# Kernel optimization log

Hardware: AMD Instinct MI355X
Metric: run time of the kernel (lower is better)

## Reference

```python
import jax, jax.numpy as jnp
import numpy as np
from jax import lax

T, B, N_IN, N_HID = 4096, 2048, 1, 32


def setup_inputs() -> dict:
    key = jax.random.key(0)
    ks = jax.random.split(key, 7)
    s_ih = 1.0 / np.sqrt(N_HID)
    return {
        "x": jax.random.normal(ks[0], (T, B, N_IN), dtype=jnp.float32),
        "hidden": jnp.zeros((1, B, N_HID), dtype=jnp.float32),
        "W_ih": jax.random.uniform(ks[1], (N_HID, N_IN), jnp.float32, -s_ih, s_ih),
        "W_hh": jax.random.uniform(ks[2], (N_HID, N_HID), jnp.float32, -s_ih, s_ih),
        "b_ih": jax.random.uniform(ks[3], (N_HID,), jnp.float32, -s_ih, s_ih),
        "b_hh": jax.random.uniform(ks[4], (N_HID,), jnp.float32, -s_ih, s_ih),
        "W_dec": jax.random.uniform(ks[5], (N_IN, N_HID), jnp.float32, -s_ih, s_ih),
        "b_dec": jax.random.uniform(ks[6], (N_IN,), jnp.float32, -s_ih, s_ih),
    }


def reference(x, hidden, W_ih, W_hh, b_ih, b_hh, W_dec, b_dec):
    # Precompute input projection for all timesteps: [T, B, N_HID]
    x_proj = jnp.einsum("tbi,hi->tbh", x, W_ih) + b_ih + b_hh

    def step(h, xp_t):
        h_new = jax.nn.relu(xp_t + h @ W_hh.T)  # [B, N_HID]
        return h_new, h_new

    h_final, outputs = lax.scan(step, hidden[0], x_proj)  # outputs: [T, B, N_HID]
    decoded = jax.nn.sigmoid(jnp.einsum("tbh,oh->tbo", outputs, W_dec) + b_dec)
    return decoded, h_final[None]
```

## Files before the change

kernel.cpp:

```cpp
#include <hip/hip_runtime.h>
#include <math.h>


typedef float f32x2 __attribute__((ext_vector_type(2)));
typedef float f32x4 __attribute__((ext_vector_type(4)));

constexpr int T_STEPS = 4096;
constexpr int BATCH   = 2048;
constexpr int NH      = 32;

template <int CTRL>
__device__ __forceinline__ float dpp_f(float v) {
    return __builtin_bit_cast(float, __builtin_amdgcn_update_dpp(
        0, __builtin_bit_cast(int, v), CTRL, 0xf, 0xf, true));
}

__global__ __launch_bounds__(64) void rnn_fused_kernel(
    const float* __restrict__ x,
    const float* __restrict__ hidden,
    const float* __restrict__ W_ih,
    const float* __restrict__ W_hh,
    const float* __restrict__ b_ih,
    const float* __restrict__ b_hh,
    const float* __restrict__ W_dec,
    const float* __restrict__ b_dec,
    float* __restrict__ out)
{
    __shared__ __align__(16) float hbuf[NH];

    const int lane = threadIdx.x;
    const int i    = lane & 31;
    const int kh   = lane >> 5;
    const int b    = blockIdx.x;

    const float wih  = W_ih[i];
    const float cb   = b_ih[i] + b_hh[i];
    const float wih0 = kh ? 0.0f : wih;
    const float cb0  = kh ? 0.0f : cb;
    const float wdec = W_dec[i];
    const float bdec = b_dec[0];

    f32x2 w[8];
    #pragma unroll
    for (int j = 0; j < 4; ++j) {
        f32x4 v = *(const f32x4*)(W_hh + i * NH + kh * 16 + 4 * j);
        w[2*j]   = f32x2{v.x, v.y};
        w[2*j+1] = f32x2{v.z, v.w};
    }

    hbuf[i] = hidden[b * NH + i];

    const float* xb = x + b;
    float xr[8];
    #pragma unroll
    for (int j = 0; j < 8; ++j) xr[j] = xb[(size_t)j * BATCH];

    float* outd = out + b;
    constexpr float NLOG2E = -1.44269504088896340736f;
    const f32x4* hp = (const f32x4*)hbuf + 4 * kh;
    float h = 0.0f;

    for (int t0 = 0; t0 < T_STEPS; t0 += 8) {
        const int tn = (t0 + 8 <= T_STEPS - 8) ? (t0 + 8) : (T_STEPS - 8);
        const float* xnb = xb + (size_t)tn * BATCH;
        float xn[8];
        #pragma unroll
        for (int j = 0; j < 8; ++j) xn[j] = xnb[(size_t)j * BATCH];

        #pragma unroll
        for (int j = 0; j < 8; ++j) {
            const f32x4 h0 = hp[0], h1 = hp[1], h2 = hp[2], h3 = hp[3];

            f32x2 a0 = f32x2{fmaf(xr[j], wih0, cb0), 0.0f};
            f32x2 a1 = f32x2{0.0f, 0.0f};
            f32x2 a2 = f32x2{0.0f, 0.0f};
            f32x2 a3 = f32x2{0.0f, 0.0f};
            a0 = __builtin_elementwise_fma(f32x2{h0.x, h0.y}, w[0], a0);
            a1 = __builtin_elementwise_fma(f32x2{h0.z, h0.w}, w[1], a1);
            a2 = __builtin_elementwise_fma(f32x2{h1.x, h1.y}, w[2], a2);
            a3 = __builtin_elementwise_fma(f32x2{h1.z, h1.w}, w[3], a3);
            a0 = __builtin_elementwise_fma(f32x2{h2.x, h2.y}, w[4], a0);
            a1 = __builtin_elementwise_fma(f32x2{h2.z, h2.w}, w[5], a1);
            a2 = __builtin_elementwise_fma(f32x2{h3.x, h3.y}, w[6], a2);
            a3 = __builtin_elementwise_fma(f32x2{h3.z, h3.w}, w[7], a3);
            f32x2 s = (a0 + a1) + (a2 + a3);
            float part = s.x + s.y;

            float dot = part + __shfl_xor(part, 32, 64);
            h = fmaxf(dot, 0.0f);
            hbuf[i] = h;

            float d = h * wdec;
            d = d + dpp_f<0x111>(d);
            d = d + dpp_f<0x112>(d);
            d = d + dpp_f<0x114>(d);
            d = d + dpp_f<0x118>(d);
            d = d + dpp_f<0x142>(d);
            float z  = d + bdec;
            float e  = __builtin_amdgcn_exp2f(z * NLOG2E);
            float sg = __builtin_amdgcn_rcpf(1.0f + e);
            if (lane == 31) outd[(size_t)(t0 + j) * BATCH] = sg;

            xr[j] = xn[j];
        }
    }

    if (lane < 32)
        out[(size_t)T_STEPS * BATCH + (size_t)b * NH + i] = h;
}

extern "C" void kernel_launch(void* const* d_in, const int* in_sizes, int n_in,
                              void* d_out, int out_size, void* d_ws, size_t ws_size,
                              hipStream_t stream) {
    const float* x      = (const float*)d_in[0];
    const float* hidden = (const float*)d_in[1];
    const float* W_ih   = (const float*)d_in[2];
    const float* W_hh   = (const float*)d_in[3];
    const float* b_ih   = (const float*)d_in[4];
    const float* b_hh   = (const float*)d_in[5];
    const float* W_dec  = (const float*)d_in[6];
    const float* b_dec  = (const float*)d_in[7];
    float* out          = (float*)d_out;

    dim3 grid(BATCH);
    dim3 block(64);
    hipLaunchKernelGGL(rnn_fused_kernel, grid, block, 0, stream,
                       x, hidden, W_ih, W_hh, b_ih, b_hh, W_dec, b_dec, out);
}
```

Baseline: 923.2 us.

## Replace LDS hidden-state broadcast with DPP row-rotate register matvec

Removes the shared-memory hbuf round trip for the recurrent state. The 32x32 matvec is now computed with DPP row_ror rotations across 16-lane rows, using per-lane pre-permuted weights and a runtime check of rotation direction. Partial sums are combined with ds_swizzle, and the new state is routed between half-waves with shfl_xor. The intent is to shorten the per-step serial latency (LDS write, then read) of the recurrence, in exchange for more cross-lane ops and extra shuffles per step.

```diff
diff --git a/kernel.cpp b/kernel.cpp
--- a/kernel.cpp
+++ b/kernel.cpp
@@ -1,9 +1,6 @@
 #include <hip/hip_runtime.h>
 #include <math.h>
 
-
-typedef float f32x2 __attribute__((ext_vector_type(2)));
-typedef float f32x4 __attribute__((ext_vector_type(4)));
 
 constexpr int T_STEPS = 4096;
 constexpr int BATCH   = 2048;
@@ -26,29 +23,30 @@
     const float* __restrict__ b_dec,
     float* __restrict__ out)
 {
-    __shared__ __align__(16) float hbuf[NH];
-
     const int lane = threadIdx.x;
-    const int i    = lane & 31;
+    const int p    = lane & 15;
+    const int row  = (lane >> 4) & 1;
     const int kh   = lane >> 5;
+    const int o    = (kh << 4) | p;
     const int b    = blockIdx.x;
 
-    const float wih  = W_ih[i];
-    const float cb   = b_ih[i] + b_hh[i];
-    const float wih0 = kh ? 0.0f : wih;
-    const float cb0  = kh ? 0.0f : cb;
-    const float wdec = W_dec[i];
+    const float wih0 = row ? 0.0f : W_ih[o];
+    const float cb0  = row ? 0.0f : (b_ih[o] + b_hh[o]);
+    const float wdO  = W_dec[o];
     const float bdec = b_dec[0];
 
-    f32x2 w[8];
+    int rot1 = __builtin_amdgcn_update_dpp(0, p, 0x121, 0xf, 0xf, true);
+    const bool minus = (rot1 == ((p - 1) & 15));
+
+    float wK[16];
     #pragma unroll
-    for (int j = 0; j < 4; ++j) {
-        f32x4 v = *(const f32x4*)(W_hh + i * NH + kh * 16 + 4 * j);
-        w[2*j]   = f32x2{v.x, v.y};
-        w[2*j+1] = f32x2{v.z, v.w};
+    for (int r = 0; r < 16; ++r) {
+        int q = minus ? ((p - r) & 15) : ((p + r) & 15);
+        wK[r] = W_hh[o * NH + (row << 4) + q];
     }
 
-    hbuf[i] = hidden[b * NH + i];
+    float hk = hidden[b * NH + (row << 4) + p];
+    const bool keep = (row == kh);
 
     const float* xb = x + b;
     float xr[8];
@@ -57,8 +55,6 @@
 
     float* outd = out + b;
     constexpr float NLOG2E = -1.44269504088896340736f;
-    const f32x4* hp = (const f32x4*)hbuf + 4 * kh;
-    float h = 0.0f;
 
     for (int t0 = 0; t0 < T_STEPS; t0 += 8) {
         const int tn = (t0 + 8 <= T_STEPS - 8) ? (t0 + 8) : (T_STEPS - 8);
@@ -69,44 +65,51 @@
 
         #pragma unroll
         for (int j = 0; j < 8; ++j) {
-            const f32x4 h0 = hp[0], h1 = hp[1], h2 = hp[2], h3 = hp[3];
+            float a0 = fmaf(xr[j], wih0, cb0);
+            a0 = fmaf(hk, wK[0], a0);
+            float a1 = 0.0f;
+            a1 = fmaf(dpp_f<0x121>(hk), wK[ 1], a1);
+            a0 = fmaf(dpp_f<0x122>(hk), wK[ 2], a0);
+            a1 = fmaf(dpp_f<0x123>(hk), wK[ 3], a1);
+            a0 = fmaf(dpp_f<0x124>(hk), wK[ 4], a0);
+            a1 = fmaf(dpp_f<0x125>(hk), wK[ 5], a1);
+            a0 = fmaf(dpp_f<0x126>(hk), wK[ 6], a0);
+            a1 = fmaf(dpp_f<0x127>(hk), wK[ 7], a1);
+            a0 = fmaf(dpp_f<0x128>(hk), wK[ 8], a0);
+            a1 = fmaf(dpp_f<0x129>(hk), wK[ 9], a1);
+            a0 = fmaf(dpp_f<0x12A>(hk), wK[10], a0);
+            a1 = fmaf(dpp_f<0x12B>(hk), wK[11], a1);
+            a0 = fmaf(dpp_f<0x12C>(hk), wK[12], a0);
+            a1 = fmaf(dpp_f<0x12D>(hk), wK[13], a1);
+            a0 = fmaf(dpp_f<0x12E>(hk), wK[14], a0);
+            a1 = fmaf(dpp_f<0x12F>(hk), wK[15], a1);
+            float P = a0 + a1;
 
-            f32x2 a0 = f32x2{fmaf(xr[j], wih0, cb0), 0.0f};
-            f32x2 a1 = f32x2{0.0f, 0.0f};
-            f32x2 a2 = f32x2{0.0f, 0.0f};
-            f32x2 a3 = f32x2{0.0f, 0.0f};
-            a0 = __builtin_elementwise_fma(f32x2{h0.x, h0.y}, w[0], a0);
-            a1 = __builtin_elementwise_fma(f32x2{h0.z, h0.w}, w[1], a1);
-            a2 = __builtin_elementwise_fma(f32x2{h1.x, h1.y}, w[2], a2);
-            a3 = __builtin_elementwise_fma(f32x2{h1.z, h1.w}, w[3], a3);
-            a0 = __builtin_elementwise_fma(f32x2{h2.x, h2.y}, w[4], a0);
-            a1 = __builtin_elementwise_fma(f32x2{h2.z, h2.w}, w[5], a1);
-            a2 = __builtin_elementwise_fma(f32x2{h3.x, h3.y}, w[6], a2);
-            a3 = __builtin_elementwise_fma(f32x2{h3.z, h3.w}, w[7], a3);
-            f32x2 s = (a0 + a1) + (a2 + a3);
-            float part = s.x + s.y;
+            float Pp = __builtin_bit_cast(float, __builtin_amdgcn_ds_swizzle(
+                __builtin_bit_cast(int, P), 0x401F));
+            float dot = P + Pp;
+            float hO  = fmaxf(dot, 0.0f);
 
-            float dot = part + __shfl_xor(part, 32, 64);
-            h = fmaxf(dot, 0.0f);
-            hbuf[i] = h;
+            float hx = __shfl_xor(hO, 32, 64);
+            hk = keep ? hO : hx;
 
-            float d = h * wdec;
+            float d = hO * wdO;
             d = d + dpp_f<0x111>(d);
             d = d + dpp_f<0x112>(d);
             d = d + dpp_f<0x114>(d);
             d = d + dpp_f<0x118>(d);
-            d = d + dpp_f<0x142>(d);
-            float z  = d + bdec;
+            float dx = __shfl_xor(d, 32, 64);
+            float z  = (d + dx) + bdec;
             float e  = __builtin_amdgcn_exp2f(z * NLOG2E);
             float sg = __builtin_amdgcn_rcpf(1.0f + e);
-            if (lane == 31) outd[(size_t)(t0 + j) * BATCH] = sg;
+            if (lane == 15) outd[(size_t)(t0 + j) * BATCH] = sg;
 
             xr[j] = xn[j];
         }
     }
 
     if (lane < 32)
-        out[(size_t)T_STEPS * BATCH + (size_t)b * NH + i] = h;
+        out[(size_t)T_STEPS * BATCH + (size_t)b * NH + (lane & 31)] = hk;
 }
 
 extern "C" void kernel_launch(void* const* d_in, const int* in_sizes, int n_in,
```

Result: slower. 1.059 ms (+14.7%).
